# Kernel optimization log

Measured on AMD Instinct MI355X. Metric: run time of the kernel, lower is better.

## Reference

```python
import jax, jax.numpy as jnp
import numpy as np

N, C, D, T, V = 64, 64, 64, 300, 25  # batch, in_ch, out_ch, time, joints
EPS = 1e-5

def _shift(c, sign):
    i = np.arange(V)[:, None]
    j = np.arange(c)[None, :]
    return jnp.asarray(((i * c + j + sign * j * c) % (c * V)).reshape(-1).astype(np.int32))

def hardswish(x):
    return x * jnp.clip(x + 3.0, 0.0, 6.0) * (1.0 / 6.0)

def bn3(x, g, b):
    # BatchNorm1d on (n, ch, L): stats over (batch, length), training-mode batch stats
    m = x.mean((0, 2), keepdims=True)
    v = x.var((0, 2), keepdims=True)
    return g[None, :, None] * (x - m) * jax.lax.rsqrt(v + EPS) + b[None, :, None]

def setup_inputs():
    key = jax.random.key(0)
    ks = jax.random.split(key, 8)
    r = lambda k, s, sc=0.05: jax.random.normal(k, s, jnp.float32) * sc
    return {
        'x0': jax.random.normal(ks[0], (N, C, T, V), jnp.float32),
        'shift_in': _shift(C, +1),
        'shift_out': _shift(D, -1),
        'Wv': r(ks[1], (1, V)), 'bv': jnp.zeros((1,), jnp.float32),
        'gv': jnp.ones((1,), jnp.float32), 'bev': jnp.zeros((1,), jnp.float32),
        'Wt': r(ks[2], (1, T)), 'bt': jnp.zeros((1,), jnp.float32),
        'gt': jnp.ones((1,), jnp.float32), 'bet': jnp.zeros((1,), jnp.float32),
        'Ws': r(ks[3], (D, C)), 'bs': jnp.zeros((D,), jnp.float32),
        'gs': jnp.ones((D,), jnp.float32), 'bes': jnp.zeros((D,), jnp.float32),
        'Wv2': r(ks[4], (C, D)), 'bv2': jnp.zeros((C,), jnp.float32),
        'Wt2': r(ks[5], (D, D)), 'bt2': jnp.zeros((D,), jnp.float32),
        'Lw': r(ks[6], (C, D), (1.0 / D) ** 0.5), 'Lb': jnp.zeros((1, 1, D), jnp.float32),
        'gbn': jnp.ones((V * D,), jnp.float32), 'bbn': jnp.zeros((V * D,), jnp.float32),
    }

def _forward(x0, Wv, bv, gv, bev, Wt, bt, gt, bet, Ws, bs, gs, bes,
             Wv2, bv2, Wt2, bt2, Lw, Lb, gbn, bbn, shift_in, shift_out):
    n, c, t, v = x0.shape
    d = Lw.shape[1]
    # shift-in gather over flattened (v*c) columns
    x = x0.transpose(0, 2, 3, 1).reshape(n * t, v * c)[:, shift_in]
    x = x.reshape(n, t, v, c).transpose(0, 3, 1, 2)  # (n,c,t,v)
    # --- YczAtt ---
    xv = x.transpose(0, 3, 1, 2).reshape(n, v, c * t)        # (n,v,c*t)
    xv = hardswish(bn3(jnp.einsum('ov,nvl->nol', Wv, xv) + bv[:, None], gv, bev))
    xt = x.transpose(0, 2, 1, 3).reshape(n, t, c * v)        # (n,t,c*v)
    xt = hardswish(bn3(jnp.einsum('ot,ntl->nol', Wt, xt) + bt[:, None], gt, bet))
    xs = jnp.concatenate([xt, xv], axis=2).reshape(n, c, t + v)
    xs = hardswish(bn3(jnp.einsum('oc,ncl->nol', Ws, xs) + bs[:, None], gs, bes))
    x_time = xs[:, :, :t]                                    # (n,d,t)
    x_view = xs[:, :, t:]                                    # (n,d,v)
    x_time = (jnp.einsum('od,ndl->nol', Wt2, x_time) + bt2[:, None]).mean(0, keepdims=True)
    x_view = (jnp.einsum('cd,ndl->ncl', Wv2, x_view) + bv2[:, None]).mean(0, keepdims=True)
    x_time = jax.nn.sigmoid(x_time)                          # (1,d,t)
    x_view = jax.nn.sigmoid(x_view).transpose(0, 2, 1)       # (1,v,c)
    # --- gate + linear + shift-out + BN + residual ---
    xm = x.transpose(0, 2, 3, 1).reshape(n * t, v, c)
    xm = xm * (jnp.tanh(x_view) + 1.0)
    y = jnp.einsum('nwc,cd->nwd', xm, Lw) + Lb               # (n*t,v,d)
    y = y.reshape(n * t, v * d)[:, shift_out]
    m = y.mean(0)
    var = y.var(0)
    y = gbn * (y - m) * jax.lax.rsqrt(var + EPS) + bbn
    y = y.reshape(n, t, v, d).transpose(0, 3, 1, 2)          # (n,d,t,v)
    y = jax.nn.relu(y + x0)                                  # down = identity (c == d)
    return y, x_time

def reference(x0, shift_in, shift_out, Wv, bv, gv, bev, Wt, bt, gt, bet,
              Ws, bs, gs, bes, Wv2, bv2, Wt2, bt2, Lw, Lb, gbn, bbn):
    return _forward(x0, Wv, bv, gv, bev, Wt, bt, gt, bet, Ws, bs, gs, bes,
                    Wv2, bv2, Wt2, bt2, Lw, Lb, gbn, bbn, shift_in, shift_out)
```

## Files before the change

kernel.cpp:

```cpp
#include <hip/hip_runtime.h>

typedef unsigned short u16;
typedef unsigned int   u32;

#define EPSF 1e-5f

typedef __attribute__((ext_vector_type(8))) short bf16x8;
typedef __attribute__((ext_vector_type(4))) float f32x4;

__device__ __forceinline__ u16 f2us(float f){
  union { float f; u32 i; } v; v.f = f;
  u32 i = v.i;
  return (u16)((i + 0x7FFFu + ((i >> 16) & 1u)) >> 16);
}
__device__ __forceinline__ float us2f(u16 u){
  union { u32 i; float f; } v; v.i = ((u32)u) << 16; return v.f;
}
__device__ __forceinline__ float hswish(float x){
  return x * fminf(fmaxf(x + 3.f, 0.f), 6.f) * (1.f/6.f);
}
__device__ __forceinline__ float sigm(float x){ return 1.f / (1.f + expf(-x)); }

#define WS_PARTIAL 0
#define WS_XV      0
#define WS_XT      1228800
#define WS_XS      1331200
#define WS_S       2662400
#define WS_GATE    2683200
#define WS_PART1   2684800
#define WS_ACCXS   2685056
#define WS_COLSTAT 2685184
#define WS_ABN     2688384
#define WS_BBN     2689984

__global__ __launch_bounds__(256) void k_zero(float* p, int cnt){
  int i = blockIdx.x*256 + threadIdx.x;
  if (i < cnt) p[i] = 0.f;
}

__global__ __launch_bounds__(256) void k1(const float* __restrict__ x0,
    const float* __restrict__ Wv, const float* __restrict__ bv,
    const float* __restrict__ Wt, const float* __restrict__ bt,
    float* __restrict__ ws)
{
  __shared__ float slab[7500];
  __shared__ float wvc[25];
  __shared__ float wts[300];
  __shared__ float colS[25];
  __shared__ float red[8];
  int blk = blockIdx.x;
  int c = blk & 63;
  int tid = threadIdx.x;
  const float4* src = (const float4*)(x0) + blk*1875;
  float4* dst = (float4*)slab;
  for (int i = tid; i < 1875; i += 256) dst[i] = src[i];
  int cm = c % 25;
  if (tid < 25){ wvc[tid] = Wv[(tid - cm + 25) % 25]; colS[tid] = 0.f; }
  for (int i = tid; i < 300; i += 256) wts[i] = Wt[i];
  __syncthreads();
  float bvf = bv[0];
  float s1 = 0.f, s2 = 0.f;
  float ca[25];
  #pragma unroll
  for (int u = 0; u < 25; u++) ca[u] = 0.f;
  for (int t = tid; t < 300; t += 256){
    const float* row = &slab[t*25];
    float wt = wts[t];
    float xv = bvf;
    #pragma unroll
    for (int u = 0; u < 25; u++){
      float xf = row[u];
      xv += wvc[u] * xf;
      ca[u] += wt * xf;
    }
    ws[WS_XV + blk*300 + t] = xv;
    s1 += xv; s2 += xv*xv;
  }
  #pragma unroll
  for (int off = 32; off >= 1; off >>= 1){
    s1 += __shfl_xor(s1, off);
    s2 += __shfl_xor(s2, off);
    #pragma unroll
    for (int u = 0; u < 25; u++) ca[u] += __shfl_xor(ca[u], off);
  }
  int lane = tid & 63, wvi = tid >> 6;
  if (lane == 0){
    #pragma unroll
    for (int u = 0; u < 25; u++) atomicAdd(&colS[u], ca[u]);
    red[wvi] = s1; red[4 + wvi] = s2;
  }
  __syncthreads();
  if (wvi == 0){
    float btf = bt[0];
    float val = 0.f;
    if (lane < 25){
      val = colS[(lane + cm) % 25] + btf;
      ws[WS_XT + blk*25 + lane] = val;
    }
    float t1 = val, t2 = val*val;
    #pragma unroll
    for (int off = 32; off >= 1; off >>= 1){ t1 += __shfl_xor(t1, off); t2 += __shfl_xor(t2, off); }
    if (lane == 0){
      float* slot = &ws[WS_PART1 + (blk & 63)*4];
      atomicAdd(slot+0, red[0]+red[1]+red[2]+red[3]);
      atomicAdd(slot+1, red[4]+red[5]+red[6]+red[7]);
      atomicAdd(slot+2, t1);
      atomicAdd(slot+3, t2);
    }
  }
}

__global__ __launch_bounds__(256) void k2(
    const float* __restrict__ Ws_, const float* __restrict__ gv, const float* __restrict__ bev,
    const float* __restrict__ gt, const float* __restrict__ bet,
    float* __restrict__ ws)
{
  __shared__ float xsc[64*82];
  __shared__ float wsl[64*65];
  __shared__ float accs[128];
  __shared__ float bnp[4];
  int tid = threadIdx.x;
  int n = blockIdx.x >> 2;
  int chunk = blockIdx.x & 3;
  int l0 = chunk * 82;
  int cw = (325 - l0 < 82) ? (325 - l0) : 82;
  if (tid < 64){
    float p0 = ws[WS_PART1 + tid*4 + 0];
    float p1 = ws[WS_PART1 + tid*4 + 1];
    float p2 = ws[WS_PART1 + tid*4 + 2];
    float p3 = ws[WS_PART1 + tid*4 + 3];
    #pragma unroll
    for (int off = 32; off >= 1; off >>= 1){
      p0 += __shfl_xor(p0, off); p1 += __shfl_xor(p1, off);
      p2 += __shfl_xor(p2, off); p3 += __shfl_xor(p3, off);
    }
    if (tid == 0){
      float Mv = 1228800.f;
      float mv = p0 / Mv;
      float varv = p1 / Mv - mv*mv;
      float av = gv[0] * rsqrtf(varv + EPSF);
      bnp[0] = av; bnp[1] = bev[0] - mv*av;
      float Mt = 102400.f;
      float mt = p2 / Mt;
      float vart = p3 / Mt - mt*mt;
      float at = gt[0] * rsqrtf(vart + EPSF);
      bnp[2] = at; bnp[3] = bet[0] - mt*at;
    }
  }
  for (int i = tid; i < 4096; i += 256){
    int o = i >> 6, cc = i & 63;
    wsl[o*65 + cc] = Ws_[i];
  }
  if (tid < 128) accs[tid] = 0.f;
  __syncthreads();
  float a_v = bnp[0], b_v = bnp[1], a_t = bnp[2], b_t = bnp[3];
  for (int i = tid; i < 64*cw; i += 256){
    int ch = i / cw, li = i - ch*cw;
    int f = ch*325 + l0 + li;
    float e;
    if (f < 1600) e = ws[WS_XT + n*1600 + f] * a_t + b_t;
    else          e = ws[WS_XV + n*19200 + (f - 1600)] * a_v + b_v;
    xsc[ch*82 + li] = hswish(e);
  }
  __syncthreads();
  int o = tid & 63;
  float s1 = 0.f, s2 = 0.f;
  for (int i = tid; i < 64*cw; i += 256){
    int li = i >> 6;
    float acc = 0.f;
    #pragma unroll 8
    for (int cc = 0; cc < 64; cc++)
      acc += wsl[o*65 + cc] * xsc[cc*82 + li];
    ws[WS_XS + (n*64 + o)*325 + l0 + li] = acc;
    s1 += acc; s2 += acc*acc;
  }
  atomicAdd(&accs[o*2+0], s1);
  atomicAdd(&accs[o*2+1], s2);
  __syncthreads();
  if (tid < 128) atomicAdd(&ws[WS_ACCXS + tid], accs[tid]);
}

__global__ __launch_bounds__(256) void k3(const float* __restrict__ gs, const float* __restrict__ bes,
                                          float* __restrict__ ws)
{
  int i = blockIdx.x*256 + threadIdx.x;
  if (i >= 20800) return;
  int dch = i / 325, l = i - dch*325;
  float s1 = ws[WS_ACCXS + dch*2], s2 = ws[WS_ACCXS + dch*2 + 1];
  float m = s1 / 20800.f;
  float var = s2 / 20800.f - m*m;
  float a = gs[dch] * rsqrtf(var + EPSF);
  float b = bes[dch] - m*a;
  float sum = 0.f;
  for (int n = 0; n < 64; n++)
    sum += hswish(ws[WS_XS + (n*64 + dch)*325 + l] * a + b);
  ws[WS_S + i] = sum;
}

__global__ __launch_bounds__(256) void k4(const float* __restrict__ Wt2, const float* __restrict__ bt2,
    const float* __restrict__ Wv2, const float* __restrict__ bv2,
    float* __restrict__ out2, float* __restrict__ ws)
{
  int i = blockIdx.x*256 + threadIdx.x;
  if (i < 19200){
    int o = i / 300, t = i - o*300;
    float acc = 0.f;
    #pragma unroll 8
    for (int dd = 0; dd < 64; dd++)
      acc += Wt2[o*64+dd] * ws[WS_S + dd*325 + t];
    out2[i] = sigm(acc * (1.f/64.f) + bt2[o]);
  } else if (i < 20800){
    int g = i - 19200;
    int v = g >> 6, cc = g & 63;
    float acc = 0.f;
    #pragma unroll 8
    for (int dd = 0; dd < 64; dd++)
      acc += Wv2[cc*64+dd] * ws[WS_S + dd*325 + 300 + v];
    ws[WS_GATE + v*64 + cc] = tanhf(sigm(acc * (1.f/64.f) + bv2[cc])) + 1.f;
  }
}

__global__ __launch_bounds__(512, 2) void k5(const float* __restrict__ x0,
    const float* __restrict__ Lw, float* __restrict__ ws)
{
  __shared__ u16 xraw[64*154];
  __shared__ u16 zsh[160*72];
  __shared__ u16 lwt[64*72];
  __shared__ float gate[1600];
  __shared__ float colacc[3300];
  int tid = threadIdx.x;
  int n = blockIdx.x >> 3, e8 = blockIdx.x & 7;
  int c0 = (e8*50) >> 3, c1 = ((e8+1)*50) >> 3;
  const float2* xsrc = (const float2*)x0;

  for (int i = tid; i < 1600; i += 512) gate[i] = ws[WS_GATE + i];
  for (int i = tid; i < 4096; i += 512){
    int c = i >> 6, d = i & 63;
    lwt[d*72 + c] = f2us(Lw[c*64 + d]);
  }
  for (int i = tid; i < 3300; i += 512) colacc[i] = 0.f;
  for (int i = tid; i < 640; i += 512){ int c = i & 63, r = 150 + (i >> 6); zsh[r*72 + c] = 0; }
  for (int i = tid; i < 4800; i += 512){
    int c = i / 75, j = i - c*75;
    float2 xy = xsrc[(n*64 + c)*3750 + c0*75 + j];
    *(u32*)&xraw[c*154 + 2*j] = (u32)f2us(xy.x) | ((u32)f2us(xy.y) << 16);
  }

  u32 gsrc[10]; int gadr[10];
  #pragma unroll
  for (int k = 0; k < 10; k++){
    int p = tid + k*512;
    if (k < 9 || p < 4800){
      int cp = (p & 31)*2, r = p >> 5;
      int v = r - 25*((r*41) >> 10);
      int base = r - v;
      int w = v + cp;
      int u1 = w - 25*((w*41) >> 10);
      int w2 = w + 1;
      int u2 = w2 - 25*((w2*41) >> 10);
      gsrc[k] = (u32)(cp*154 + base + u1) | ((u32)((cp+1)*154 + base + u2) << 16);
      gadr[k] = v*64 + cp;
    }
  }

  int lane = tid & 63, wvi = tid >> 6;
  int m16 = lane & 15, kq = lane >> 4;
  int dd = (wvi & 3)*16 + m16;
  bf16x8 b0, b1;
  float s_acc[20], q_acc[20];
  #pragma unroll
  for (int z = 0; z < 20; z++){ s_acc[z] = 0.f; q_acc[z] = 0.f; }

  for (int cc = c0; cc < c1; cc++){
    __syncthreads();
    #pragma unroll
    for (int k = 0; k < 10; k++){
      if (k < 9 || tid < 192){
        int p = tid + k*512;
        int dst = (p >> 5)*72 + (p & 31)*2;
        float gA = gate[gadr[k]];
        float gB = gate[gadr[k] + 1];
        u16 x1 = xraw[gsrc[k] & 0xFFFFu];
        u16 x2 = xraw[gsrc[k] >> 16];
        u32 pk = (u32)f2us(us2f(x1)*gA) | ((u32)f2us(us2f(x2)*gB) << 16);
        *(u32*)&zsh[dst] = pk;
      }
    }
    __syncthreads();
    if (cc == c0){
      b0 = *(const bf16x8*)&lwt[dd*72 + kq*8];
      b1 = *(const bf16x8*)&lwt[dd*72 + 32 + kq*8];
    }
    float2 pf[10];
    bool has = (cc + 1 < c1);
    if (has){
      #pragma unroll
      for (int k = 0; k < 10; k++){
        int i = tid + k*512;
        if (i < 4800){
          int c = i / 75, j = i - c*75;
          pf[k] = xsrc[(n*64 + c)*3750 + (cc+1)*75 + j];
        }
      }
    }
    #pragma unroll
    for (int it = 0; it < 5; it++){
      int T = wvi + it*8;
      int r0 = (T >> 2) * 16;
      bf16x8 a0 = *(const bf16x8*)&zsh[(r0 + m16)*72 + kq*8];
      bf16x8 a1 = *(const bf16x8*)&zsh[(r0 + m16)*72 + 32 + kq*8];
      f32x4 a = {0.f,0.f,0.f,0.f};
      a = __builtin_amdgcn_mfma_f32_16x16x32_bf16(a0, b0, a, 0, 0, 0);
      a = __builtin_amdgcn_mfma_f32_16x16x32_bf16(a1, b1, a, 0, 0, 0);
      #pragma unroll
      for (int q = 0; q < 4; q++){
        float y = a[q];
        s_acc[it*4 + q] += y;
        q_acc[it*4 + q] += y*y;
      }
    }
    if (has){
      #pragma unroll
      for (int k = 0; k < 10; k++){
        int i = tid + k*512;
        if (i < 4800){
          int c = i / 75, j = i - c*75;
          *(u32*)&xraw[c*154 + 2*j] = (u32)f2us(pf[k].x) | ((u32)f2us(pf[k].y) << 16);
        }
      }
    }
  }
  #pragma unroll
  for (int it = 0; it < 5; it++){
    int T = wvi + it*8;
    int r0 = (T >> 2) * 16;
    #pragma unroll
    for (int q = 0; q < 4; q++){
      int r = r0 + kq*4 + q;
      if (r < 150){
        int v = r - 25*((r*41) >> 10);
        atomicAdd(&colacc[v*66 + dd], s_acc[it*4 + q]);
        atomicAdd(&colacc[1650 + v*66 + dd], q_acc[it*4 + q]);
      }
    }
  }
  __syncthreads();
  float* dst = ws + WS_PARTIAL + blockIdx.x*3200;
  for (int i = tid; i < 3200; i += 512){
    int f = (i < 1600) ? i : (i - 1600);
    int v = f >> 6, d = f & 63;
    dst[i] = colacc[((i < 1600) ? 0 : 1650) + v*66 + d];
  }
}

__global__ __launch_bounds__(256) void k5a(float* __restrict__ ws)
{
  __shared__ float red[256];
  int tid = threadIdx.x;
  int f = blockIdx.x*64 + (tid & 63);
  int bsub = tid >> 6;
  const float* src = ws + WS_PARTIAL + f;
  float acc = 0.f;
  #pragma unroll 8
  for (int b = bsub; b < 512; b += 4)
    acc += src[b*3200];
  red[tid] = acc;
  __syncthreads();
  if (tid < 64){
    float t = red[tid] + red[tid+64] + red[tid+128] + red[tid+192];
    ws[WS_COLSTAT + f] = t;
  }
}

__global__ __launch_bounds__(256) void k5b(const float* __restrict__ gbn, const float* __restrict__ bbn,
                                           float* __restrict__ ws)
{
  int i = blockIdx.x*256 + threadIdx.x;
  if (i >= 1600) return;
  int v = i >> 6, d = i & 63;
  float s = ws[WS_COLSTAT + i], q = ws[WS_COLSTAT + 1600 + i];
  float m = s / 19200.f;
  float var = q / 19200.f - m*m;
  float rs = rsqrtf(var + EPSF);
  int vi = (v + d) % 25;
  int f = vi*64 + d;
  float a = gbn[f] * rs;
  ws[WS_ABN + i] = a;
  ws[WS_BBN + i] = bbn[f] - m*a;
}

__global__ __launch_bounds__(512, 2) void k6(const float* __restrict__ x0,
    const float* __restrict__ Lw, float* __restrict__ out, float* __restrict__ ws)
{
  __shared__ u16 xraw[64*154];
  __shared__ u16 zsh[160*72];
  __shared__ u16 lwt[64*72];
  __shared__ float gate[1600];
  __shared__ float affA[1650];
  __shared__ float affB[1650];
  int tid = threadIdx.x;
  int n = blockIdx.x >> 3, e8 = blockIdx.x & 7;
  int c0 = (e8*50) >> 3, c1 = ((e8+1)*50) >> 3;
  const float2* xsrc = (const float2*)x0;

  for (int i = tid; i < 1600; i += 512){
    gate[i] = ws[WS_GATE + i];
    int v = i >> 6, d = i & 63;
    affA[v*66 + d] = ws[WS_ABN + i];
    affB[v*66 + d] = ws[WS_BBN + i];
  }
  for (int i = tid; i < 4096; i += 512){
    int c = i >> 6, d = i & 63;
    lwt[d*72 + c] = f2us(Lw[c*64 + d]);
  }
  for (int i = tid; i < 640; i += 512){ int c = i & 63, r = 150 + (i >> 6); zsh[r*72 + c] = 0; }
  for (int i = tid; i < 4800; i += 512){
    int c = i / 75, j = i - c*75;
    float2 xy = xsrc[(n*64 + c)*3750 + c0*75 + j];
    *(u32*)&xraw[c*154 + 2*j] = (u32)f2us(xy.x) | ((u32)f2us(xy.y) << 16);
  }

  u32 gsrc[10]; int gadr[10];
  #pragma unroll
  for (int k = 0; k < 10; k++){
    int p = tid + k*512;
    if (k < 9 || p < 4800){
      int cp = (p & 31)*2, r = p >> 5;
      int v = r - 25*((r*41) >> 10);
      int base = r - v;
      int w = v + cp;
      int u1 = w - 25*((w*41) >> 10);
      int w2 = w + 1;
      int u2 = w2 - 25*((w2*41) >> 10);
      gsrc[k] = (u32)(cp*154 + base + u1) | ((u32)((cp+1)*154 + base + u2) << 16);
      gadr[k] = v*64 + cp;
    }
  }

  int lane = tid & 63, wvi = tid >> 6;
  int m16 = lane & 15, kq = lane >> 4;
  int dd = (wvi & 3)*16 + m16;

  u32 eidx[20];
  #pragma unroll
  for (int it = 0; it < 5; it++){
    int T = wvi + it*8;
    int r0 = (T >> 2) * 16;
    #pragma unroll
    for (int q = 0; q < 4; q++){
      int r = r0 + kq*4 + q;
      u32 e = 0xFFFFu;
      if (r < 150){
        int v = r - 25*((r*41) >> 10);
        int w = v + dd;
        int u = w - 25*((w*41) >> 10);
        e = (u32)(dd*154 + (r - v) + u) | ((u32)(v*66 + dd) << 16);
      }
      eidx[it*4 + q] = e;
    }
  }

  bf16x8 b0, b1;

  for (int cc = c0; cc < c1; cc++){
    __syncthreads();
    #pragma unroll
    for (int k = 0; k < 10; k++){
      if (k < 9 || tid < 192){
        int p = tid + k*512;
        int dst = (p >> 5)*72 + (p & 31)*2;
        float gA = gate[gadr[k]];
        float gB = gate[gadr[k] + 1];
        u16 x1 = xraw[gsrc[k] & 0xFFFFu];
        u16 x2 = xraw[gsrc[k] >> 16];
        u32 pk = (u32)f2us(us2f(x1)*gA) | ((u32)f2us(us2f(x2)*gB) << 16);
        *(u32*)&zsh[dst] = pk;
      }
    }
    __syncthreads();
    if (cc == c0){
      b0 = *(const bf16x8*)&lwt[dd*72 + kq*8];
      b1 = *(const bf16x8*)&lwt[dd*72 + 32 + kq*8];
    }
    float2 pf[10];
    bool has = (cc + 1 < c1);
    if (has){
      #pragma unroll
      for (int k = 0; k < 10; k++){
        int i = tid + k*512;
        if (i < 4800){
          int c = i / 75, j = i - c*75;
          pf[k] = xsrc[(n*64 + c)*3750 + (cc+1)*75 + j];
        }
      }
    }
    f32x4 acc[5];
    #pragma unroll
    for (int it = 0; it < 5; it++){
      int T = wvi + it*8;
      int r0 = (T >> 2) * 16;
      bf16x8 a0 = *(const bf16x8*)&zsh[(r0 + m16)*72 + kq*8];
      bf16x8 a1 = *(const bf16x8*)&zsh[(r0 + m16)*72 + 32 + kq*8];
      f32x4 a = {0.f,0.f,0.f,0.f};
      a = __builtin_amdgcn_mfma_f32_16x16x32_bf16(a0, b0, a, 0, 0, 0);
      a = __builtin_amdgcn_mfma_f32_16x16x32_bf16(a1, b1, a, 0, 0, 0);
      acc[it] = a;
    }
    #pragma unroll
    for (int s = 0; s < 20; s++){
      u32 e = eidx[s];
      if ((e & 0xFFFFu) != 0xFFFFu){
        int idx = (int)(e & 0xFFFFu), ao = (int)(e >> 16);
        float resid = us2f(xraw[idx]);
        float val = acc[s>>2][s&3] * affA[ao] + affB[ao] + resid;
        xraw[idx] = f2us(fmaxf(val, 0.f));
      }
    }
    __syncthreads();
    for (int i = tid; i < 4800; i += 512){
      int d = i / 75, j = i - d*75;
      u32 pk = *(const u32*)&xraw[d*154 + 2*j];
      float2 o; o.x = us2f((u16)(pk & 0xFFFFu)); o.y = us2f((u16)(pk >> 16));
      ((float2*)out)[(n*64 + d)*3750 + cc*75 + j] = o;
    }
    __syncthreads();
    if (has){
      #pragma unroll
      for (int k = 0; k < 10; k++){
        int i = tid + k*512;
        if (i < 4800){
          int c = i / 75, j = i - c*75;
          *(u32*)&xraw[c*154 + 2*j] = (u32)f2us(pf[k].x) | ((u32)f2us(pf[k].y) << 16);
        }
      }
    }
  }
}

extern "C" void kernel_launch(void* const* d_in, const int* in_sizes, int n_in,
                              void* d_out, int out_size, void* d_ws, size_t ws_size,
                              hipStream_t stream)
{
  const float* x0  = (const float*)d_in[0];
  const float* Wv  = (const float*)d_in[3];
  const float* bv  = (const float*)d_in[4];
  const float* gv  = (const float*)d_in[5];
  const float* bev = (const float*)d_in[6];
  const float* Wt  = (const float*)d_in[7];
  const float* bt  = (const float*)d_in[8];
  const float* gt  = (const float*)d_in[9];
  const float* bet = (const float*)d_in[10];
  const float* Ws_ = (const float*)d_in[11];
  const float* gs  = (const float*)d_in[13];
  const float* bes = (const float*)d_in[14];
  const float* Wv2 = (const float*)d_in[15];
  const float* bv2 = (const float*)d_in[16];
  const float* Wt2 = (const float*)d_in[17];
  const float* bt2 = (const float*)d_in[18];
  const float* Lw  = (const float*)d_in[19];
  const float* gbn = (const float*)d_in[21];
  const float* bbn = (const float*)d_in[22];
  float* out = (float*)d_out;
  float* ws = (float*)d_ws;

  k_zero<<<dim3(14), dim3(256), 0, stream>>>(ws + WS_PART1, 3584);
  k1<<<dim3(4096), dim3(256), 0, stream>>>(x0, Wv, bv, Wt, bt, ws);
  k2<<<dim3(256), dim3(256), 0, stream>>>(Ws_, gv, bev, gt, bet, ws);
  k3<<<dim3(82), dim3(256), 0, stream>>>(gs, bes, ws);
  k4<<<dim3(82), dim3(256), 0, stream>>>(Wt2, bt2, Wv2, bv2, out + 30720000, ws);
  k5<<<dim3(512), dim3(512), 0, stream>>>(x0, Lw, ws);
  k5a<<<dim3(50), dim3(256), 0, stream>>>(ws);
  k5b<<<dim3(7), dim3(256), 0, stream>>>(gbn, bbn, ws);
  k6<<<dim3(512), dim3(512), 0, stream>>>(x0, Lw, out, ws);
}
```

Baseline: 492.8 us.

## Store bf16 pre-BN outputs in workspace and apply BN with a streaming kernel

The stats pass now writes the shifted, gated linear output y as bf16 into a workspace buffer, reusing the xraw tile as a staging area. A new elementwise kernel then applies the BN affine, adds the residual and applies ReLU, replacing the second pass that recomputed the gather and MFMA. The k3 reduction over batch is also split across 8 y-blocks using atomicAdd to raise parallelism. In exchange it adds about 61MB of workspace traffic plus an extra sync per iteration in k5, and the path is only taken when the workspace is large enough.

```diff
diff --git a/kernel.cpp b/kernel.cpp
--- a/kernel.cpp
+++ b/kernel.cpp
@@ -32,6 +32,7 @@
 #define WS_COLSTAT 2685184
 #define WS_ABN     2688384
 #define WS_BBN     2689984
+#define WS_YWS     2692096
 
 __global__ __launch_bounds__(256) void k_zero(float* p, int cnt){
   int i = blockIdx.x*256 + threadIdx.x;
@@ -192,9 +193,10 @@
   float a = gs[dch] * rsqrtf(var + EPSF);
   float b = bes[dch] - m*a;
   float sum = 0.f;
-  for (int n = 0; n < 64; n++)
+  int n0 = blockIdx.y * 8;
+  for (int n = n0; n < n0 + 8; n++)
     sum += hswish(ws[WS_XS + (n*64 + dch)*325 + l] * a + b);
-  ws[WS_S + i] = sum;
+  atomicAdd(&ws[WS_S + i], sum);
 }
 
 __global__ __launch_bounds__(256) void k4(const float* __restrict__ Wt2, const float* __restrict__ bt2,
@@ -220,8 +222,8 @@
   }
 }
 
-__global__ __launch_bounds__(512, 2) void k5(const float* __restrict__ x0,
-    const float* __restrict__ Lw, float* __restrict__ ws)
+__global__ __launch_bounds__(512, 2) void k5y(const float* __restrict__ x0,
+    const float* __restrict__ Lw, float* __restrict__ ws, const int storeY)
 {
   __shared__ u16 xraw[64*154];
   __shared__ u16 zsh[160*72];
@@ -232,6 +234,7 @@
   int n = blockIdx.x >> 3, e8 = blockIdx.x & 7;
   int c0 = (e8*50) >> 3, c1 = ((e8+1)*50) >> 3;
   const float2* xsrc = (const float2*)x0;
+  u32* yws = (u32*)(ws + WS_YWS);
 
   for (int i = tid; i < 1600; i += 512) gate[i] = ws[WS_GATE + i];
   for (int i = tid; i < 4096; i += 512){
@@ -266,6 +269,26 @@
   int lane = tid & 63, wvi = tid >> 6;
   int m16 = lane & 15, kq = lane >> 4;
   int dd = (wvi & 3)*16 + m16;
+
+  u32 eidx[20];
+  #pragma unroll
+  for (int it = 0; it < 5; it++){
+    int T = wvi + it*8;
+    int r0 = (T >> 2) * 16;
+    #pragma unroll
+    for (int q = 0; q < 4; q++){
+      int r = r0 + kq*4 + q;
+      u32 e = 0xFFFFu;
+      if (r < 150){
+        int v = r - 25*((r*41) >> 10);
+        int w = v + dd;
+        int u = w - 25*((w*41) >> 10);
+        e = (u32)(dd*154 + (r - v) + u);
+      }
+      eidx[it*4 + q] = e;
+    }
+  }
+
   bf16x8 b0, b1;
   float s_acc[20], q_acc[20];
   #pragma unroll
@@ -303,6 +326,7 @@
         }
       }
     }
+    f32x4 acc[5];
     #pragma unroll
     for (int it = 0; it < 5; it++){
       int T = wvi + it*8;
@@ -312,6 +336,7 @@
       f32x4 a = {0.f,0.f,0.f,0.f};
       a = __builtin_amdgcn_mfma_f32_16x16x32_bf16(a0, b0, a, 0, 0, 0);
       a = __builtin_amdgcn_mfma_f32_16x16x32_bf16(a1, b1, a, 0, 0, 0);
+      acc[it] = a;
       #pragma unroll
       for (int q = 0; q < 4; q++){
         float y = a[q];
@@ -319,6 +344,19 @@
         q_acc[it*4 + q] += y*y;
       }
     }
+    if (storeY){
+      #pragma unroll
+      for (int s = 0; s < 20; s++){
+        u32 e = eidx[s];
+        if (e != 0xFFFFu) xraw[e] = f2us(acc[s>>2][s&3]);
+      }
+      __syncthreads();
+      for (int i = tid; i < 4800; i += 512){
+        int d = i / 75, j = i - d*75;
+        yws[(n*64 + d)*3750 + cc*75 + j] = *(const u32*)&xraw[d*154 + 2*j];
+      }
+    }
+    __syncthreads();
     if (has){
       #pragma unroll
       for (int k = 0; k < 10; k++){
@@ -373,7 +411,7 @@
 }
 
 __global__ __launch_bounds__(256) void k5b(const float* __restrict__ gbn, const float* __restrict__ bbn,
-                                           float* __restrict__ ws)
+                                           float* __restrict__ ws, const int rot)
 {
   int i = blockIdx.x*256 + threadIdx.x;
   if (i >= 1600) return;
@@ -385,8 +423,35 @@
   int vi = (v + d) % 25;
   int f = vi*64 + d;
   float a = gbn[f] * rs;
-  ws[WS_ABN + i] = a;
-  ws[WS_BBN + i] = bbn[f] - m*a;
+  int o = rot ? (vi*64 + d) : i;
+  ws[WS_ABN + o] = a;
+  ws[WS_BBN + o] = bbn[f] - m*a;
+}
+
+__global__ __launch_bounds__(256) void k6n(const float* __restrict__ x0,
+    float* __restrict__ out, const float* __restrict__ ws)
+{
+  __shared__ float sA[25];
+  __shared__ float sB[25];
+  int row = blockIdx.x;
+  int d = row & 63;
+  int tid = threadIdx.x;
+  if (tid < 25)       sA[tid]      = ws[WS_ABN + tid*64 + d];
+  else if (tid < 50)  sB[tid - 25] = ws[WS_BBN + (tid - 25)*64 + d];
+  __syncthreads();
+  const u32*    yrow = (const u32*)(ws + WS_YWS) + row*3750;
+  const float2* xrow = (const float2*)x0 + row*3750;
+  float2*       orow = (float2*)out + row*3750;
+  for (int j = tid; j < 3750; j += 256){
+    u32 pk = yrow[j];
+    float2 xv = xrow[j];
+    int u0 = (2*j) % 25;
+    int u1 = (u0 == 24) ? 0 : (u0 + 1);
+    float2 o;
+    o.x = fmaxf(us2f((u16)(pk & 0xFFFFu)) * sA[u0] + sB[u0] + xv.x, 0.f);
+    o.y = fmaxf(us2f((u16)(pk >> 16))     * sA[u1] + sB[u1] + xv.y, 0.f);
+    orow[j] = o;
+  }
 }
 
 __global__ __launch_bounds__(512, 2) void k6(const float* __restrict__ x0,
@@ -563,13 +628,20 @@
   float* out = (float*)d_out;
   float* ws = (float*)d_ws;
 
+  const int big = (ws_size >= (size_t)(WS_YWS + 15360000) * 4) ? 1 : 0;
+
   k_zero<<<dim3(14), dim3(256), 0, stream>>>(ws + WS_PART1, 3584);
+  k_zero<<<dim3(82), dim3(256), 0, stream>>>(ws + WS_S, 20800);
   k1<<<dim3(4096), dim3(256), 0, stream>>>(x0, Wv, bv, Wt, bt, ws);
   k2<<<dim3(256), dim3(256), 0, stream>>>(Ws_, gv, bev, gt, bet, ws);
-  k3<<<dim3(82), dim3(256), 0, stream>>>(gs, bes, ws);
+  k3<<<dim3(82, 8), dim3(256), 0, stream>>>(gs, bes, ws);
   k4<<<dim3(82), dim3(256), 0, stream>>>(Wt2, bt2, Wv2, bv2, out + 30720000, ws);
-  k5<<<dim3(512), dim3(512), 0, stream>>>(x0, Lw, ws);
+  k5y<<<dim3(512), dim3(512), 0, stream>>>(x0, Lw, ws, big);
   k5a<<<dim3(50), dim3(256), 0, stream>>>(ws);
-  k5b<<<dim3(7), dim3(256), 0, stream>>>(gbn, bbn, ws);
-  k6<<<dim3(512), dim3(512), 0, stream>>>(x0, Lw, out, ws);
-}
+  k5b<<<dim3(7), dim3(256), 0, stream>>>(gbn, bbn, ws, big);
+  if (big){
+    k6n<<<dim3(4096), dim3(256), 0, stream>>>(x0, out, ws);
+  } else {
+    k6<<<dim3(512), dim3(512), 0, stream>>>(x0, Lw, out, ws);
+  }
+}
```

Result: no change. 488.6 us (-0.9%).
